# Optimization experiments

Measured on AMD Instinct MI355X. Metric: run time of the kernel, lower is better.

Reference implementation:

```python
import jax, jax.numpy as jnp
import numpy as np

FRACTION_BITS = 16
INTEGER_BITS = 16


def round_to_fixed(x):
    # floor-quantize to 2^-16 steps, clamp to signed 16-bit integer range
    delta = 2.0 ** (-FRACTION_BITS)
    bound = 2.0 ** (INTEGER_BITS - 1)
    return jnp.clip(jnp.floor(x / delta) * delta, -bound, bound - 1.0)


def setup_inputs() -> dict:
    key = jax.random.key(0)
    k1, k2, k3, k4 = jax.random.split(key, 4)
    N, IN_F, OUT_F = 4096, 4096, 4096
    inp = jax.random.normal(k1, (N, IN_F), dtype=jnp.float32)
    # reset_parameters: shift ~ U(-10,-1), sign ~ U(-1,0), bias ~ U(-b,b), b=1/sqrt(fan_in)
    shift = jax.random.uniform(k2, (OUT_F, IN_F), minval=-10.0, maxval=-1.0, dtype=jnp.float32)
    sign = jax.random.uniform(k3, (OUT_F, IN_F), minval=-1.0, maxval=0.0, dtype=jnp.float32)
    b = 1.0 / np.sqrt(IN_F)
    bias = jax.random.uniform(k4, (OUT_F,), minval=-b, maxval=b, dtype=jnp.float32)
    return {"input": inp, "shift": shift, "sign": sign, "bias": bias}


def reference(input, shift, sign, bias):
    # eager (non-kernel) path of LinearShiftFunction.forward
    q_in = round_to_fixed(input)
    q_bias = round_to_fixed(bias)
    s = jnp.clip(sign, -1.0, 1.0)
    v = jnp.exp2(jnp.round(shift)) * jnp.sign(s)  # [out_f, in_f] power-of-two weights
    out = q_in @ v.T + q_bias[None, :]
    return out
```

## Files before the change

kernel.cpp:

```cpp
#include <hip/hip_runtime.h>
#include <hip/hip_bf16.h>


#define BM 256
#define BN 256
#define BK 64

typedef __bf16 bf16_t;
typedef __attribute__((ext_vector_type(8))) __bf16 bf16x8;
typedef __attribute__((ext_vector_type(4))) __bf16 bf16x4;
typedef __attribute__((ext_vector_type(4))) float f32x4;

__device__ __forceinline__ float q16(float x) {
    float f = floorf(x * 65536.0f) * (1.0f / 65536.0f);
    return fminf(fmaxf(f, -32768.0f), 32767.0f);
}

__global__ void quant_input_kernel(const float* __restrict__ in,
                                   bf16_t* __restrict__ out, int nvec) {
    int stride = gridDim.x * blockDim.x;
    for (int i = blockIdx.x * blockDim.x + threadIdx.x; i < nvec; i += stride) {
        float4 v = reinterpret_cast<const float4*>(in)[i];
        bf16x4 o;
        o[0] = (bf16_t)q16(v.x);
        o[1] = (bf16_t)q16(v.y);
        o[2] = (bf16_t)q16(v.z);
        o[3] = (bf16_t)q16(v.w);
        reinterpret_cast<bf16x4*>(out)[i] = o;
    }
}

__global__ void make_weight_kernel(const float* __restrict__ shift,
                                   const float* __restrict__ sign_,
                                   bf16_t* __restrict__ out, int nvec) {
    int stride = gridDim.x * blockDim.x;
    for (int i = blockIdx.x * blockDim.x + threadIdx.x; i < nvec; i += stride) {
        float4 sh = reinterpret_cast<const float4*>(shift)[i];
        float4 sg = reinterpret_cast<const float4*>(sign_)[i];
        float shs[4] = {sh.x, sh.y, sh.z, sh.w};
        float sgs[4] = {sg.x, sg.y, sg.z, sg.w};
        bf16x4 o;
#pragma unroll
        for (int j = 0; j < 4; ++j) {
            float s = fminf(fmaxf(sgs[j], -1.0f), 1.0f);
            float sv = (s > 0.0f) ? 1.0f : ((s < 0.0f) ? -1.0f : 0.0f);
            o[j] = (bf16_t)(exp2f(rintf(shs[j])) * sv);
        }
        reinterpret_cast<bf16x4*>(out)[i] = o;
    }
}


#define VMW(N) asm volatile("s_waitcnt vmcnt(" #N ")" ::: "memory")
#define BARF() do { __builtin_amdgcn_s_barrier(); asm volatile("" ::: "memory"); } while (0)

#define STAGE(LDSOFF, SRC) do {                                                          \
    const bf16_t* _s = (SRC);                                                            \
    bf16_t* _d = &lds[(LDSOFF)] + tid * 8;                                               \
    __builtin_amdgcn_global_load_lds((const __attribute__((address_space(1))) void*)_s,  \
                                     (__attribute__((address_space(3))) void*)_d,        \
                                     16, 0, 0);                                          \
    __builtin_amdgcn_global_load_lds(                                                    \
        (const __attribute__((address_space(1))) void*)(_s + (size_t)64 * K),            \
        (__attribute__((address_space(3))) void*)(_d + 4096), 16, 0, 0);                 \
} while (0)

#define READ_A(BUF, MH) do {                                                             \
    const bf16_t* _As = &lds[(BUF) * 32768 + wm * 8192];                                 \
    _Pragma("unroll") for (int m = 0; m < 4; ++m)                                        \
        _Pragma("unroll") for (int kk = 0; kk < 2; ++kk)                                 \
            af[m][kk] = *(const bf16x8*)&_As[((MH) * 64 + m * 16 + fr) * 64 +            \
                                             ((((kk << 2) | hi) ^ fr7) << 3)];           \
} while (0)

#define READ_B(BUF, NH, BF) do {                                                         \
    const bf16_t* _Bs = &lds[(BUF) * 32768 + 16384 + (wn >> 1) * 8192];                  \
    _Pragma("unroll") for (int n = 0; n < 2; ++n)                                        \
        _Pragma("unroll") for (int kk = 0; kk < 2; ++kk)                                 \
            BF[n][kk] = *(const bf16x8*)&_Bs[((wn & 1) * 64 + ((NH) * 2 + n) * 16 + fr)  \
                                                 * 64 +                                  \
                                             ((((kk << 2) | hi) ^ fr7) << 3)];           \
} while (0)

#define QUAD(MH, NH, BF) do {                                                            \
    _Pragma("unroll") for (int m = 0; m < 4; ++m)                                        \
        _Pragma("unroll") for (int n = 0; n < 2; ++n)                                    \
            _Pragma("unroll") for (int kk = 0; kk < 2; ++kk)                             \
                acc[(MH) * 4 + m][(NH) * 2 + n] =                                        \
                    __builtin_amdgcn_mfma_f32_16x16x32_bf16(                             \
                        af[m][kk], BF[n][kk], acc[(MH) * 4 + m][(NH) * 2 + n], 0, 0, 0); \
} while (0)

#define MFMA_PH(MH, NH, BF)                                                              \
    __builtin_amdgcn_s_setprio(1);                                                       \
    QUAD(MH, NH, BF);                                                                    \
    __builtin_amdgcn_s_setprio(0);

#define TILE(BUF, T, S, ENDW) do {                                                      \
                                                                            \
    READ_A(BUF, 0);                                                                      \
    READ_B(BUF, 0, b0f);                                                                 \
    BARF();                                                                              \
    MFMA_PH(0, 0, b0f)                                                                   \
    BARF();                                                                              \
                                                                            \
    READ_B(BUF, 1, b1f);                                                                 \
    BARF();                                                                              \
    MFMA_PH(0, 1, b1f)                                                                   \
    BARF();                                                                              \
                        \
    READ_A(BUF, 1);                                                                      \
    if (S) {                                                                             \
        STAGE((BUF) * 32768 + 2 * 8192, srcB0 + (size_t)((T) + 2) * 64);                 \
        STAGE((BUF) * 32768 + 3 * 8192, srcB1 + (size_t)((T) + 2) * 64);                 \
    }                                                                                    \
    BARF();                                                                              \
    MFMA_PH(1, 0, b0f)                                                                   \
    BARF();                                                                              \
                                    \
    if (S) {                                                                             \
        STAGE((BUF) * 32768 + 0 * 8192, srcA0 + (size_t)((T) + 2) * 64);                 \
        STAGE((BUF) * 32768 + 1 * 8192, srcA1 + (size_t)((T) + 2) * 64);                 \
    }                                                                                    \
    BARF();                                                                              \
    MFMA_PH(1, 1, b1f)                                                                   \
    if ((ENDW) == 8) VMW(8);                                                             \
    else if ((ENDW) == 0) VMW(0);                                                        \
    BARF();                                                                              \
} while (0)

__global__ __launch_bounds__(512, 2)
void gemm256_kernel(const bf16_t* __restrict__ A,
                    const bf16_t* __restrict__ B,
                    const float* __restrict__ bias,
                    float* __restrict__ C,
                    int M, int N, int K) {
    __shared__ bf16_t lds[65536];

    const int ntn = N / BN;
    const int nwg = gridDim.x;
    const int q = nwg >> 3, r = nwg & 7;
    const int xcd = blockIdx.x & 7, lid = blockIdx.x >> 3;
    const int swz = (xcd < r ? xcd * (q + 1) : r * (q + 1) + (xcd - r) * q) + lid;
    const int tile_m = (swz / ntn) * BM;
    const int tile_n = (swz % ntn) * BN;

    const int tid = threadIdx.x;
    const int lane = tid & 63;
    const int wid = tid >> 6;
    const int wm = wid >> 2;
    const int wn = wid & 3;
    const int fr = lane & 15;
    const int hi = lane >> 4;
    const int fr7 = fr & 7;

    const int colsrc_e = ((((tid & 7) * 16) ^ ((tid & 56) << 1)) >> 1);
    const bf16_t* srcA0 = A + (size_t)(tile_m + (tid >> 3)) * K + colsrc_e;
    const bf16_t* srcA1 = srcA0 + (size_t)128 * K;
    const bf16_t* srcB0 = B + (size_t)(tile_n + (tid >> 3)) * K + colsrc_e;
    const bf16_t* srcB1 = srcB0 + (size_t)128 * K;

    bf16x8 af[4][2], b0f[2][2], b1f[2][2];
    f32x4 acc[8][4] = {};

    STAGE(16384, srcB0);
    STAGE(24576, srcB1);
    STAGE(0, srcA0);
    STAGE(8192, srcA1);
    STAGE(32768 + 16384, srcB0 + 64);
    STAGE(32768 + 24576, srcB1 + 64);
    STAGE(32768 + 0, srcA0 + 64);
    STAGE(32768 + 8192, srcA1 + 64);
    VMW(8);
    BARF();

    const int npairs = K / 128;
    for (int i = 0; i < npairs - 1; ++i) {
        TILE(0, 2 * i, 1, 8);
        TILE(1, 2 * i + 1, 1, 8);
    }
    TILE(0, 2 * npairs - 2, 0, 0);
    TILE(1, 2 * npairs - 1, 0, -1);

    float qb[4];
#pragma unroll
    for (int ng = 0; ng < 4; ++ng)
        qb[ng] = q16(bias[tile_n + wn * 64 + ng * 16 + fr]);
#pragma unroll
    for (int mg = 0; mg < 8; ++mg) {
        const int grow0 = tile_m + wm * 128 + mg * 16 + hi * 4;
#pragma unroll
        for (int ng = 0; ng < 4; ++ng) {
            const int gcol = tile_n + wn * 64 + ng * 16 + fr;
#pragma unroll
            for (int rr = 0; rr < 4; ++rr)
                C[(size_t)(grow0 + rr) * N + gcol] = acc[mg][ng][rr] + qb[ng];
        }
    }
}

extern "C" void kernel_launch(void* const* d_in, const int* in_sizes, int n_in,
                              void* d_out, int out_size, void* d_ws, size_t ws_size,
                              hipStream_t stream) {
    const float* inp   = (const float*)d_in[0];
    const float* shift = (const float*)d_in[1];
    const float* sign_ = (const float*)d_in[2];
    const float* bias  = (const float*)d_in[3];
    float* out = (float*)d_out;

    const int OUT_F = in_sizes[3];
    const int IN_F  = in_sizes[1] / OUT_F;
    const int Mrows = in_sizes[0] / IN_F;

    bf16_t* Aq = (bf16_t*)d_ws;
    bf16_t* Wq = Aq + (size_t)Mrows * IN_F;

    const int nA = Mrows * IN_F;
    const int nW = OUT_F * IN_F;

    quant_input_kernel<<<2048, 256, 0, stream>>>(inp, Aq, nA >> 2);
    make_weight_kernel<<<2048, 256, 0, stream>>>(shift, sign_, Wq, nW >> 2);

    dim3 grid((Mrows / BM) * (OUT_F / BN));
    gemm256_kernel<<<grid, 512, 0, stream>>>(Aq, Wq, bias, out,
                                             Mrows, OUT_F, IN_F);
}
```

Baseline: 166.1 us.

## Restage GEMM pipeline: spread global-to-LDS loads and prefetch next B fragments

Reorganizes the per-tile schedule of the 256x256 bf16 GEMM so global_load_lds stages are spread across all four MFMA phases. Some stages now target the other LDS buffer for tile T+1. The first B fragment of the next tile is read from LDS during the last phase of the current one. Explicit lgkmcnt waits and sched_barriers replace implicit ordering, and vmcnt waits are retuned per tile, including new prologue and epilogue variants. The aim is to hide LDS read and global load latency behind MFMAs, at the cost of fragile hand-tuned wait counts that could cause races if any count is wrong.

```diff
diff --git a/kernel.cpp b/kernel.cpp
--- a/kernel.cpp
+++ b/kernel.cpp
@@ -52,6 +52,8 @@
 
 
 #define VMW(N) asm volatile("s_waitcnt vmcnt(" #N ")" ::: "memory")
+#define LGKM(N) asm volatile("s_waitcnt lgkmcnt(" #N ")" ::: "memory")
+#define SBAR0() __builtin_amdgcn_sched_barrier(0)
 #define BARF() do { __builtin_amdgcn_s_barrier(); asm volatile("" ::: "memory"); } while (0)
 
 #define STAGE(LDSOFF, SRC) do {                                                          \
@@ -96,36 +98,36 @@
     QUAD(MH, NH, BF);                                                                    \
     __builtin_amdgcn_s_setprio(0);
 
-#define TILE(BUF, T, S, ENDW) do {                                                      \
-                                                                            \
+#define TILE(BUF, T, S01, S23, W2, W3, PF) do {                                          \
+                         \
     READ_A(BUF, 0);                                                                      \
-    READ_B(BUF, 0, b0f);                                                                 \
-    BARF();                                                                              \
+    READ_B(BUF, 1, b1f);                                                                 \
+    if (S01) STAGE(((BUF) ^ 1) * 32768 + 3 * 8192, srcB1 + (size_t)((T) + 1) * 64);      \
+    BARF();                                                                              \
+    LGKM(4); SBAR0();                                                                    \
     MFMA_PH(0, 0, b0f)                                                                   \
     BARF();                                                                              \
-                                                                            \
-    READ_B(BUF, 1, b1f);                                                                 \
-    BARF();                                                                              \
+                        \
+    if (S01) STAGE(((BUF) ^ 1) * 32768 + 1 * 8192, srcA1 + (size_t)((T) + 1) * 64);      \
+    BARF();                                                                              \
+    LGKM(0); SBAR0();                                                                    \
     MFMA_PH(0, 1, b1f)                                                                   \
     BARF();                                                                              \
-                        \
+                                                       \
     READ_A(BUF, 1);                                                                      \
-    if (S) {                                                                             \
-        STAGE((BUF) * 32768 + 2 * 8192, srcB0 + (size_t)((T) + 2) * 64);                 \
-        STAGE((BUF) * 32768 + 3 * 8192, srcB1 + (size_t)((T) + 2) * 64);                 \
-    }                                                                                    \
-    BARF();                                                                              \
+    if (S23) STAGE((BUF) * 32768 + 2 * 8192, srcB0 + (size_t)((T) + 2) * 64);            \
+    BARF();                                                                              \
+    LGKM(0); SBAR0();                                                                    \
     MFMA_PH(1, 0, b0f)                                                                   \
-    BARF();                                                                              \
-                                    \
-    if (S) {                                                                             \
-        STAGE((BUF) * 32768 + 0 * 8192, srcA0 + (size_t)((T) + 2) * 64);                 \
-        STAGE((BUF) * 32768 + 1 * 8192, srcA1 + (size_t)((T) + 2) * 64);                 \
-    }                                                                                    \
-    BARF();                                                                              \
+    VMW(W2);                                                                             \
+    BARF();                                                                              \
+                            \
+    if (PF) READ_B((BUF) ^ 1, 0, b0f);                                                   \
+    if (S23) STAGE((BUF) * 32768 + 0 * 8192, srcA0 + (size_t)((T) + 2) * 64);            \
+    BARF();                                                                              \
+    LGKM(4); SBAR0();                                                                    \
     MFMA_PH(1, 1, b1f)                                                                   \
-    if ((ENDW) == 8) VMW(8);                                                             \
-    else if ((ENDW) == 0) VMW(0);                                                        \
+    VMW(W3);                                                                             \
     BARF();                                                                              \
 } while (0)
 
@@ -168,19 +170,22 @@
     STAGE(0, srcA0);
     STAGE(8192, srcA1);
     STAGE(32768 + 16384, srcB0 + 64);
+    STAGE(32768 + 0, srcA0 + 64);
     STAGE(32768 + 24576, srcB1 + 64);
-    STAGE(32768 + 0, srcA0 + 64);
     STAGE(32768 + 8192, srcA1 + 64);
     VMW(8);
     BARF();
+    READ_B(0, 0, b0f);
 
     const int npairs = K / 128;
-    for (int i = 0; i < npairs - 1; ++i) {
-        TILE(0, 2 * i, 1, 8);
-        TILE(1, 2 * i + 1, 1, 8);
-    }
-    TILE(0, 2 * npairs - 2, 0, 0);
-    TILE(1, 2 * npairs - 1, 0, -1);
+    TILE(0, 0, 0, 1, 8, 4, 1);
+    TILE(1, 1, 1, 1, 8, 4, 1);
+    for (int i = 1; i < npairs - 1; ++i) {
+        TILE(0, 2 * i, 1, 1, 8, 4, 1);
+        TILE(1, 2 * i + 1, 1, 1, 8, 4, 1);
+    }
+    TILE(0, 2 * npairs - 2, 1, 0, 6, 0, 1);
+    TILE(1, 2 * npairs - 1, 0, 0, 63, 63, 0);
 
     float qb[4];
 #pragma unroll
```

After: 167.9 us. About the same (+1.1%).
